# Kernel optimization log

Hardware: AMD Instinct MI355X
Metric: run time of the kernel (lower is better)

Reference implementation:

```python
import jax, jax.numpy as jnp
import numpy as np

# BiDiGemma (Aveygo/SRNext) wrapping RecurrentGemma-style ResidualBlocks:
#   block0 = RECURRENT (causal conv width 4 + RG-LRU linear recurrence)
#   block1 = local (sliding-window, MQA) ATTENTION with partial RoPE
# Dropout(0.1) is treated as eval-mode identity.

B, S, D, H = 4, 4096, 256, 4
HD = D // H            # head dim = 64
E = 3 * D              # mlp_expanded_width = expand_ratio * dim
W_ATT = D              # attention_window_size = dim = 256 (divides S)
TW = 4                 # recurrentgemma temporal conv width
_NEG = -2.3819763e38   # recurrentgemma masking constant

_PNAMES = ["ln_gamma","ln_beta","proj_w","proj_b","fconv_w","fconv_b","bconv_w","bconv_b",
 "rn0_t","rn0_c","ly_w","ly_b","lx_w","lx_b","lo_w","lo_b","c1d_w","c1d_b",
 "a_param","ig_w","ig_b","ag_w","ag_b","mlp0_up_w","mlp0_up_b","mlp0_dn_w","mlp0_dn_b",
 "rn1_t","rn1_c","q_w","k_w","v_w","o_w","o_b","mlp1_up_w","mlp1_up_b","mlp1_dn_w","mlp1_dn_b"]


def _init_params(key):
    ks = iter(jax.random.split(key, 24))
    nrm = lambda shape, s: jax.random.normal(next(ks), shape, jnp.float32) * s
    p = {}
    p["ln_gamma"] = jnp.ones((D,), jnp.float32); p["ln_beta"] = jnp.zeros((D,), jnp.float32)
    p["proj_w"] = nrm((D, D), D ** -0.5);  p["proj_b"] = jnp.zeros((D,), jnp.float32)
    p["fconv_w"] = nrm((D, D), D ** -0.5); p["fconv_b"] = jnp.zeros((D,), jnp.float32)
    p["bconv_w"] = nrm((D, D), D ** -0.5); p["bconv_b"] = jnp.zeros((D,), jnp.float32)
    p["rn0_t"] = jnp.zeros((D,), jnp.float32); p["rn0_c"] = jnp.zeros((D,), jnp.float32)
    p["ly_w"] = nrm((D, D), D ** -0.5); p["ly_b"] = jnp.zeros((D,), jnp.float32)
    p["lx_w"] = nrm((D, D), D ** -0.5); p["lx_b"] = jnp.zeros((D,), jnp.float32)
    p["lo_w"] = nrm((D, D), D ** -0.5); p["lo_b"] = jnp.zeros((D,), jnp.float32)
    p["c1d_w"] = nrm((TW, D), 0.1);     p["c1d_b"] = jnp.zeros((D,), jnp.float32)
    p["a_param"] = jnp.log(jnp.expm1(jnp.linspace(0.9, 1.5, D, dtype=jnp.float32)))
    p["ig_w"] = nrm((H, HD, HD), HD ** -0.5); p["ig_b"] = jnp.zeros((H, HD), jnp.float32)
    p["ag_w"] = nrm((H, HD, HD), HD ** -0.5); p["ag_b"] = jnp.zeros((H, HD), jnp.float32)
    p["mlp0_up_w"] = nrm((2, D, E), D ** -0.5); p["mlp0_up_b"] = jnp.zeros((2, E), jnp.float32)
    p["mlp0_dn_w"] = nrm((E, D), E ** -0.5);    p["mlp0_dn_b"] = jnp.zeros((D,), jnp.float32)
    p["rn1_t"] = jnp.zeros((D,), jnp.float32); p["rn1_c"] = jnp.zeros((D,), jnp.float32)
    p["q_w"] = nrm((D, D), D ** -0.5); p["k_w"] = nrm((D, HD), D ** -0.5); p["v_w"] = nrm((D, HD), D ** -0.5)
    p["o_w"] = nrm((D, D), D ** -0.5); p["o_b"] = jnp.zeros((D,), jnp.float32)
    p["mlp1_up_w"] = nrm((2, D, E), D ** -0.5); p["mlp1_up_b"] = jnp.zeros((2, E), jnp.float32)
    p["mlp1_dn_w"] = nrm((E, D), E ** -0.5);    p["mlp1_dn_b"] = jnp.zeros((D,), jnp.float32)
    return p


def _gelu(x):
    return jax.nn.gelu(x, approximate=False)  # torch F.gelu default (erf)


def _rms_norm(x, scale, eps=1e-6):
    var = jnp.mean(jnp.square(x), axis=-1, keepdims=True)
    return x * jax.lax.rsqrt(var + eps) * (1.0 + scale)


def _layer_norm(x, g, b, eps=1e-5):
    m = jnp.mean(x, axis=-1, keepdims=True)
    v = jnp.mean(jnp.square(x - m), axis=-1, keepdims=True)
    return (x - m) * jax.lax.rsqrt(v + eps) * g + b


def _block_diag(x, w, b):
    # BlockDiagonalLinear: per-head [HD x HD] blocks
    xh = x.reshape(*x.shape[:-1], H, HD)
    y = jnp.einsum('bshd,hdk->bshk', xh, w) + b
    return y.reshape(*x.shape)


def _causal_conv1d(x, w, b):
    # depthwise causal conv, w: [TW, D], w[TW-1] multiplies current token
    xp = jnp.pad(x, ((0, 0), (TW - 1, 0), (0, 0)))
    out = sum(xp[:, i:i + x.shape[1], :] * w[i] for i in range(TW))
    return out + b


def _rg_lru(x, pos, a_param, ig_w, ig_b, ag_w, ag_b):
    gate_x = jax.nn.sigmoid(_block_diag(x, ig_w, ig_b))
    gate_a = jax.nn.sigmoid(_block_diag(x, ag_w, ag_b))
    log_a = -8.0 * gate_a * jax.nn.softplus(a_param)   # c = 8
    a = jnp.exp(log_a)
    mult = jnp.sqrt(-jnp.expm1(2.0 * log_a))           # sqrt(1 - a^2)
    reset = (pos == 0)[..., None]
    mult = jnp.where(reset, 1.0, mult)
    bterm = x * gate_x * mult
    def comb(e1, e2):
        a1, b1 = e1
        a2, b2 = e2
        return a1 * a2, a2 * b1 + b2
    _, h = jax.lax.associative_scan(comb, (a, bterm), axis=1)
    return h


def _rope(x, pos):
    # partial RoPE: applied to first half of head dim (recurrentgemma)
    rot, rest = jnp.split(x, 2, axis=-1)
    f = rot.shape[-1] // 2
    inv_freq = 10000.0 ** (-(2.0 / rot.shape[-1]) * jnp.arange(f, dtype=jnp.float32))
    t = pos[..., None, None].astype(jnp.float32) * inv_freq  # [b, s, 1, f]
    sin, cos = jnp.sin(t), jnp.cos(t)
    x1, x2 = jnp.split(rot, 2, axis=-1)
    return jnp.concatenate([x1 * cos - x2 * sin, x2 * cos + x1 * sin, rest], axis=-1)


def _local_attention(x, pos, q_w, k_w, v_w, o_w, o_b):
    # MQA sliding-window attention, window = W_ATT; chunked to honor locality
    b, s, _ = x.shape
    q = (x @ q_w).reshape(b, s, H, HD)
    k = (x @ k_w).reshape(b, s, 1, HD)
    v = (x @ v_w).reshape(b, s, HD)
    q = _rope(q, pos) * (HD ** -0.5)
    k = _rope(k, pos)[:, :, 0]
    Wn = W_ATT
    nb = s // Wn
    qc = q.reshape(b, nb, Wn, H, HD)
    kp = jnp.pad(k, ((0, 0), (Wn, 0), (0, 0))).reshape(b, nb + 1, Wn, HD)
    vp = jnp.pad(v, ((0, 0), (Wn, 0), (0, 0))).reshape(b, nb + 1, Wn, HD)
    kc = jnp.concatenate([kp[:, :-1], kp[:, 1:]], axis=2)  # [b, nb, 2W, HD]
    vc = jnp.concatenate([vp[:, :-1], vp[:, 1:]], axis=2)
    logits = jnp.einsum('bnqhd,bnkd->bnhqk', qc, kc)
    i = jnp.arange(Wn)[:, None]
    j = jnp.arange(2 * Wn)[None, :]
    diff = (i + Wn) - j                       # q_pos - k_pos
    base = (diff >= 0) & (diff <= Wn)         # causal & q <= k + window_size
    cidx = jnp.arange(nb)[:, None, None]
    mask = base[None] & ((cidx > 0) | (j[None] >= Wn))  # no left padding in chunk 0
    logits = jnp.where(mask[None, :, None], logits, _NEG)
    probs = jax.nn.softmax(logits, axis=-1)
    out = jnp.einsum('bnhqk,bnkd->bnqhd', probs, vc).reshape(b, s, D)
    return out @ o_w + o_b


def _mlp(x, up_w, up_b, dn_w, dn_b):
    up = jnp.einsum('bsd,cde->cbse', x, up_w) + up_b[:, None, None, :]
    act = _gelu(up[0]) * up[1]
    return act @ dn_w + dn_b


def _gemma_block(x, pos, p):
    # ResidualBlock 0: RECURRENT
    raw = x
    xn = _rms_norm(raw, p['rn0_t'])
    y = _gelu(xn @ p['ly_w'] + p['ly_b'])
    xr = xn @ p['lx_w'] + p['lx_b']
    xr = _causal_conv1d(xr, p['c1d_w'], p['c1d_b'])
    xr = _rg_lru(xr, pos, p['a_param'], p['ig_w'], p['ig_b'], p['ag_w'], p['ag_b'])
    xr = (xr * y) @ p['lo_w'] + p['lo_b']
    residual = xr + raw
    x = _rms_norm(residual, p['rn0_c'])
    x = _mlp(x, p['mlp0_up_w'], p['mlp0_up_b'], p['mlp0_dn_w'], p['mlp0_dn_b']) + residual
    # ResidualBlock 1: local ATTENTION
    raw = x
    xn = _rms_norm(raw, p['rn1_t'])
    xa = _local_attention(xn, pos, p['q_w'], p['k_w'], p['v_w'], p['o_w'], p['o_b'])
    residual = xa + raw
    x = _rms_norm(residual, p['rn1_c'])
    x = _mlp(x, p['mlp1_up_w'], p['mlp1_up_b'], p['mlp1_dn_w'], p['mlp1_dn_b']) + residual
    return x


def _forward(skip, *params):
    p = dict(zip(_PNAMES, params))
    b, s, _ = skip.shape
    pos = jnp.broadcast_to(jnp.arange(s, dtype=jnp.int32)[None], (b, s))
    x = _layer_norm(skip, p['ln_gamma'], p['ln_beta']) @ p['proj_w'] + p['proj_b']
    z = jax.nn.sigmoid(jnp.mean(jax.nn.silu(skip), axis=-1, keepdims=True))
    fwd = _gemma_block(x @ p['fconv_w'] + p['fconv_b'], pos, p)  # Conv1d k=1 == pointwise
    bwd = _gemma_block(x @ p['bconv_w'] + p['bconv_b'], pos, p)
    return z * (fwd + bwd) + skip


def setup_inputs() -> dict:
    key = jax.random.key(0)
    kx, kp = jax.random.split(key)
    inp = {"skip": jax.random.normal(kx, (B, S, D), jnp.float32)}
    inp.update(_init_params(kp))
    return inp


def reference(skip, ln_gamma, ln_beta, proj_w, proj_b, fconv_w, fconv_b, bconv_w, bconv_b, rn0_t, rn0_c, ly_w, ly_b, lx_w, lx_b, lo_w, lo_b, c1d_w, c1d_b, a_param, ig_w, ig_b, ag_w, ag_b, mlp0_up_w, mlp0_up_b, mlp0_dn_w, mlp0_dn_b, rn1_t, rn1_c, q_w, k_w, v_w, o_w, o_b, mlp1_up_w, mlp1_up_b, mlp1_dn_w, mlp1_dn_b):
    return _forward(skip, ln_gamma, ln_beta, proj_w, proj_b, fconv_w, fconv_b, bconv_w, bconv_b, rn0_t, rn0_c, ly_w, ly_b, lx_w, lx_b, lo_w, lo_b, c1d_w, c1d_b, a_param, ig_w, ig_b, ag_w, ag_b, mlp0_up_w, mlp0_up_b, mlp0_dn_w, mlp0_dn_b, rn1_t, rn1_c, q_w, k_w, v_w, o_w, o_b, mlp1_up_w, mlp1_up_b, mlp1_dn_w, mlp1_dn_b)
```

## Files before the change

### kernel.cpp

```cpp
#include <hip/hip_runtime.h>
#include <math.h>
#include <stddef.h>


#define BB   4
#define SS   4096
#define DD   256
#define HH   4
#define HDIM 64
#define EE   768
#define RR   (BB*SS)
#define RR2  (2*RR)
#define WNN  256
#define CH   64
#define NCH  (SS/CH)

typedef __attribute__((ext_vector_type(8))) short bfrag;
typedef __attribute__((ext_vector_type(4))) float f4acc;

__device__ __forceinline__ float geluf(float x){
  float u = 1.5957691216f*(x + 0.044715f*x*x*x);
  float e = __expf(u);
  float t = 1.f - 2.f/(e+1.f);
  return 0.5f*x*(1.f+t);
}
__device__ __forceinline__ float sigm(float x){ return 1.0f/(1.0f+expf(-x)); }

__device__ __forceinline__ unsigned short f2bf(float x){
  unsigned u = __float_as_uint(x);
  return (unsigned short)((u + 0x7FFFu + ((u>>16)&1u)) >> 16);
}
__device__ __forceinline__ float bf2f(unsigned short h){
  return __uint_as_float(((unsigned)h) << 16);
}
__device__ __forceinline__ void split2(float v, unsigned short* h, unsigned short* l){
  unsigned short hb = f2bf(v);
  *h = hb; *l = f2bf(v - bf2f(hb));
}

__device__ __forceinline__ float wredSum(float v){
#pragma unroll
  for(int o=32;o>0;o>>=1) v += __shfl_xor(v,o,64);
  return v;
}

__global__ __launch_bounds__(256) void ln_z_k(const float* __restrict__ skip,
    const float* __restrict__ g, const float* __restrict__ b,
    unsigned short* __restrict__ oh, unsigned short* __restrict__ ol,
    float* __restrict__ z)
{
  int row  = blockIdx.x*4 + (threadIdx.x>>6);
  int lane = threadIdx.x & 63;
  float4 v = ((const float4*)(skip + (size_t)row*DD))[lane];
  float s  = v.x+v.y+v.z+v.w;
  float sq = v.x*v.x+v.y*v.y+v.z*v.z+v.w*v.w;
  float si = v.x*sigm(v.x)+v.y*sigm(v.y)+v.z*sigm(v.z)+v.w*sigm(v.w);
  s = wredSum(s); sq = wredSum(sq); si = wredSum(si);
  float mean = s*(1.0f/DD);
  float var  = sq*(1.0f/DD) - mean*mean;
  float inv  = rsqrtf(var + 1e-5f);
  float4 gv = ((const float4*)g)[lane];
  float4 bv = ((const float4*)b)[lane];
  float o0 = (v.x-mean)*inv*gv.x + bv.x;
  float o1 = (v.y-mean)*inv*gv.y + bv.y;
  float o2 = (v.z-mean)*inv*gv.z + bv.z;
  float o3 = (v.w-mean)*inv*gv.w + bv.w;
  ushort4 hi, lo;
  split2(o0,&hi.x,&lo.x); split2(o1,&hi.y,&lo.y);
  split2(o2,&hi.z,&lo.z); split2(o3,&hi.w,&lo.w);
  ((ushort4*)(oh + (size_t)row*DD))[lane] = hi;
  ((ushort4*)(ol + (size_t)row*DD))[lane] = lo;
  if(lane==0) z[row] = sigm(si*(1.0f/DD));
}

__global__ __launch_bounds__(256) void rms_k(const float* __restrict__ x,
    const float* __restrict__ t,
    unsigned short* __restrict__ oh, unsigned short* __restrict__ ol)
{
  int row  = blockIdx.x*4 + (threadIdx.x>>6);
  int lane = threadIdx.x & 63;
  float4 v = ((const float4*)(x + (size_t)row*DD))[lane];
  float sq = v.x*v.x+v.y*v.y+v.z*v.z+v.w*v.w;
  sq = wredSum(sq);
  float inv = rsqrtf(sq*(1.0f/DD) + 1e-6f);
  float4 tv = ((const float4*)t)[lane];
  float o0 = v.x*inv*(1.0f+tv.x);
  float o1 = v.y*inv*(1.0f+tv.y);
  float o2 = v.z*inv*(1.0f+tv.z);
  float o3 = v.w*inv*(1.0f+tv.w);
  ushort4 hi, lo;
  split2(o0,&hi.x,&lo.x); split2(o1,&hi.y,&lo.y);
  split2(o2,&hi.z,&lo.z); split2(o3,&hi.w,&lo.w);
  ((ushort4*)(oh + (size_t)row*DD))[lane] = hi;
  ((ushort4*)(ol + (size_t)row*DD))[lane] = lo;
}

struct TS  { const float* s; unsigned short* h; unsigned short* l; int K; int N; };
struct TS8 { TS t[8]; };

__global__ __launch_bounds__(256) void tsplit8_k(TS8 g){
  TS tt = g.t[blockIdx.y];
  int idx = blockIdx.x*256 + threadIdx.x;
  int tot = tt.K*tt.N;
  if(idx >= tot) return;
  int k = idx / tt.N;
  int n = idx - k*tt.N;
  float x = tt.s[idx];
  unsigned short hb = f2bf(x);
  unsigned short lb = f2bf(x - bf2f(hb));
  tt.h[(size_t)n*tt.K + k] = hb;
  tt.l[(size_t)n*tt.K + k] = lb;
}

template<int BN, int MODE, int DUAL, int OUT, int TERMS>
__global__ __launch_bounds__(256) void gemm_mfma(
    const unsigned short* __restrict__ Ah_g, const unsigned short* __restrict__ Al_g,
    const unsigned short* __restrict__ B0h, const unsigned short* __restrict__ B0l,
    const unsigned short* __restrict__ B1h, const unsigned short* __restrict__ B1l,
    const float* __restrict__ bias0, const float* __restrict__ bias1,
    const float* __restrict__ Res, float* __restrict__ C,
    unsigned short* __restrict__ Ch, unsigned short* __restrict__ Cl,
    int K, int lda, int ldc)
{
  constexpr int NT = BN/32;
  constexpr int ST = 40;
  __shared__ unsigned short Ash[128*ST];
  __shared__ unsigned short Asl[TERMS==3 ? 128*ST : 8];
  __shared__ unsigned short Bsh[BN*ST];
  __shared__ unsigned short Bsl[TERMS>=2 ? BN*ST : 8];
  __shared__ unsigned short B2h[DUAL?BN*ST:8];
  __shared__ unsigned short B2l[(DUAL && TERMS>=2)?BN*ST:8];

  const int tid  = threadIdx.x;
  const int lane = tid & 63, wave = tid >> 6;
  const int wm = wave >> 1, wn = wave & 1;
  const int bm = blockIdx.y*128, bn = blockIdx.x*BN;
  const int m16 = lane & 15, q = lane >> 4;

  f4acc acc[4][NT];
  f4acc acc2[DUAL?4:1][DUAL?NT:1];
#pragma unroll
  for(int i=0;i<4;i++)
#pragma unroll
    for(int j=0;j<NT;j++){
      acc[i][j] = (f4acc)0.f;
      if constexpr(DUAL) acc2[i][j] = (f4acc)0.f;
    }

  const int r0 = tid >> 2, c0 = tid & 3;
  const int coff = c0*8;
  const int d0 = r0*ST + coff, d1 = (r0+64)*ST + coff;

  const unsigned short* pAh0 = Ah_g + (size_t)(bm+r0)*lda + coff;
  const unsigned short* pAh1 = pAh0 + (size_t)64*lda;
  const unsigned short* pAl0 = (TERMS==3) ? (Al_g + (size_t)(bm+r0)*lda + coff)
                                          : (const unsigned short*)nullptr;
  const unsigned short* pAl1 = (TERMS==3) ? (pAl0 + (size_t)64*lda)
                                          : (const unsigned short*)nullptr;
  const unsigned short *pB0h0=nullptr,*pB0h1=nullptr,*pB0l0=nullptr,*pB0l1=nullptr;
  const unsigned short *pBa=nullptr,*pBb=nullptr,*pBc=nullptr,*pBd=nullptr;
  if constexpr(BN==128){
    pB0h0 = B0h + (size_t)(bn+r0)*K + coff;  pB0h1 = pB0h0 + (size_t)64*K;
    if constexpr(TERMS>=2){
      pB0l0 = B0l + (size_t)(bn+r0)*K + coff;  pB0l1 = pB0l0 + (size_t)64*K;
    }
  } else {
    pBa = B0h + (size_t)(bn+r0)*K + coff;
    if constexpr(TERMS>=2) pBb = B0l + (size_t)(bn+r0)*K + coff;
    if constexpr(DUAL){
      pBc = B1h + (size_t)(bn+r0)*K + coff;
      if constexpr(TERMS>=2) pBd = B1l + (size_t)(bn+r0)*K + coff;
    }
  }

  for(int k0 = 0; k0 < K; k0 += 32){
    *(float4*)&Ash[d0] = *(const float4*)(pAh0 + k0);
    *(float4*)&Ash[d1] = *(const float4*)(pAh1 + k0);
    if constexpr(TERMS==3){
      *(float4*)&Asl[d0] = *(const float4*)(pAl0 + k0);
      *(float4*)&Asl[d1] = *(const float4*)(pAl1 + k0);
    }
    if constexpr(BN==128){
      *(float4*)&Bsh[d0] = *(const float4*)(pB0h0 + k0);
      *(float4*)&Bsh[d1] = *(const float4*)(pB0h1 + k0);
      if constexpr(TERMS>=2){
        *(float4*)&Bsl[d0] = *(const float4*)(pB0l0 + k0);
        *(float4*)&Bsl[d1] = *(const float4*)(pB0l1 + k0);
      }
    } else {
      *(float4*)&Bsh[d0] = *(const float4*)(pBa + k0);
      if constexpr(TERMS>=2) *(float4*)&Bsl[d0] = *(const float4*)(pBb + k0);
      if constexpr(DUAL){
        *(float4*)&B2h[d0] = *(const float4*)(pBc + k0);
        if constexpr(TERMS>=2) *(float4*)&B2l[d0] = *(const float4*)(pBd + k0);
      }
    }
    __syncthreads();

    bfrag ah[4], al[TERMS==3?4:1], b0hf[NT], b0lf[TERMS>=2?NT:1];
    bfrag b1hf[DUAL?NT:1], b1lf[(DUAL&&TERMS>=2)?NT:1];
#pragma unroll
    for(int mi=0;mi<4;mi++){
      int row = wm*64 + mi*16 + m16;
      ah[mi] = *(const bfrag*)&Ash[row*ST + q*8];
      if constexpr(TERMS==3) al[mi] = *(const bfrag*)&Asl[row*ST + q*8];
    }
#pragma unroll
    for(int ni=0;ni<NT;ni++){
      int n = wn*(BN/2) + ni*16 + m16;
      b0hf[ni] = *(const bfrag*)&Bsh[n*ST + q*8];
      if constexpr(TERMS>=2) b0lf[ni] = *(const bfrag*)&Bsl[n*ST + q*8];
      if constexpr(DUAL){
        b1hf[ni] = *(const bfrag*)&B2h[n*ST + q*8];
        if constexpr(TERMS>=2) b1lf[ni] = *(const bfrag*)&B2l[n*ST + q*8];
      }
    }
#pragma unroll
    for(int mi=0;mi<4;mi++)
#pragma unroll
      for(int ni=0;ni<NT;ni++){
        acc[mi][ni] = __builtin_amdgcn_mfma_f32_16x16x32_bf16(ah[mi], b0hf[ni], acc[mi][ni],0,0,0);
        if constexpr(TERMS>=2)
          acc[mi][ni] = __builtin_amdgcn_mfma_f32_16x16x32_bf16(ah[mi], b0lf[ni], acc[mi][ni],0,0,0);
        if constexpr(TERMS==3)
          acc[mi][ni] = __builtin_amdgcn_mfma_f32_16x16x32_bf16(al[mi], b0hf[ni], acc[mi][ni],0,0,0);
        if constexpr(DUAL){
          acc2[mi][ni] = __builtin_amdgcn_mfma_f32_16x16x32_bf16(ah[mi], b1hf[ni], acc2[mi][ni],0,0,0);
          if constexpr(TERMS>=2)
            acc2[mi][ni] = __builtin_amdgcn_mfma_f32_16x16x32_bf16(ah[mi], b1lf[ni], acc2[mi][ni],0,0,0);
          if constexpr(TERMS==3)
            acc2[mi][ni] = __builtin_amdgcn_mfma_f32_16x16x32_bf16(al[mi], b1hf[ni], acc2[mi][ni],0,0,0);
        }
      }
    __syncthreads();
  }

  if constexpr(OUT==0 || OUT==1 || OUT==5){
#pragma unroll
    for(int ni=0;ni<NT;ni++){
      const int col = bn + wn*(BN/2) + ni*16 + m16;
      float bv0 = (MODE&1) ? bias0[col] : 0.f;
      float bv1 = DUAL ? bias1[col] : 0.f;
#pragma unroll
      for(int mi=0;mi<4;mi++){
#pragma unroll
        for(int r=0;r<4;r++){
          const int row = bm + wm*64 + mi*16 + q*4 + r;
          float v = acc[mi][ni][r] + bv0;
          if constexpr(DUAL){
            float v2 = acc2[mi][ni][r] + bv1;
            v = geluf(v) * v2;
          } else if(MODE&2){
            v = geluf(v);
          }
          if(MODE&8) v += Res[(size_t)row*ldc + col];
          if constexpr(OUT==0){
            C[(size_t)row*ldc + col] = v;
          } else if constexpr(OUT==1){
            unsigned short hb = f2bf(v);
            Ch[(size_t)row*ldc + col] = hb;
            Cl[(size_t)row*ldc + col] = f2bf(v - bf2f(hb));
          } else {
            Ch[(size_t)row*ldc + col] = f2bf(v);
          }
        }
      }
    }
  } else if constexpr(OUT==2){
    const int hb = bn + wn*64;
    const float p = (float)m16;
    const float invf = __expf(-p * 0.575646273248511f);
#pragma unroll
    for(int mi=0;mi<4;mi++){
#pragma unroll
      for(int r=0;r<4;r++){
        const int row = bm + wm*64 + mi*16 + q*4 + r;
        const int s = row & (SS-1);
        float t = (float)s * invf;
        float sn, cs; __sincosf(t, &sn, &cs);
        float x1 = acc[mi][0][r], x2 = acc[mi][1][r];
        float v0 = (x1*cs - x2*sn)*0.125f;
        float v1 = (x2*cs + x1*sn)*0.125f;
        float v2 = acc[mi][2][r]*0.125f;
        float v3 = acc[mi][3][r]*0.125f;
        size_t base = (size_t)row*ldc + hb;
        unsigned short hh;
        hh=f2bf(v0); Ch[base+m16]=hh;    Cl[base+m16]   =f2bf(v0-bf2f(hh));
        hh=f2bf(v1); Ch[base+16+m16]=hh; Cl[base+16+m16]=f2bf(v1-bf2f(hh));
        hh=f2bf(v2); Ch[base+32+m16]=hh; Cl[base+32+m16]=f2bf(v2-bf2f(hh));
        hh=f2bf(v3); Ch[base+48+m16]=hh; Cl[base+48+m16]=f2bf(v3-bf2f(hh));
      }
    }
  } else if constexpr(OUT==3){
    const float p = (float)m16;
    const float invf = __expf(-p * 0.575646273248511f);
#pragma unroll
    for(int mi=0;mi<4;mi++){
#pragma unroll
      for(int r=0;r<4;r++){
        const int row = bm + wm*64 + mi*16 + q*4 + r;
        const int s = row & (SS-1);
        float v0, v1;
        if(wn==0){
          float t = (float)s * invf;
          float sn, cs; __sincosf(t, &sn, &cs);
          float x1 = acc[mi][0][r], x2 = acc[mi][1][r];
          v0 = x1*cs - x2*sn;
          v1 = x2*cs + x1*sn;
        } else {
          v0 = acc[mi][0][r]; v1 = acc[mi][1][r];
        }
        size_t base = (size_t)row*ldc + wn*32;
        unsigned short hh;
        hh=f2bf(v0); Ch[base+m16]=hh;    Cl[base+m16]   =f2bf(v0-bf2f(hh));
        hh=f2bf(v1); Ch[base+16+m16]=hh; Cl[base+16+m16]=f2bf(v1-bf2f(hh));
      }
    }
  } else if constexpr(OUT==4){
#pragma unroll
    for(int ni=0;ni<NT;ni++){
      const int col = wn*32 + ni*16 + m16;
#pragma unroll
      for(int mi=0;mi<4;mi++){
        const int rowb = bm + wm*64 + mi*16 + q*4;
        const int b = rowb >> 12, sl = rowb & (SS-1);
        ushort4 hv;
        hv.x = f2bf(acc[mi][ni][0]); hv.y = f2bf(acc[mi][ni][1]);
        hv.z = f2bf(acc[mi][ni][2]); hv.w = f2bf(acc[mi][ni][3]);
        *(ushort4*)(Ch + ((size_t)(b*64 + col))*SS + sl) = hv;
      }
    }
  }
}

__global__ __launch_bounds__(256) void gates_k(
    const float* __restrict__ X,
    const float* __restrict__ igw, const float* __restrict__ igb,
    const float* __restrict__ agw, const float* __restrict__ agb,
    const float* __restrict__ ap,
    float* __restrict__ Aout, float* __restrict__ Bout)
{
  constexpr int BK = 16;
  __shared__ float Ask[BK][132];
  __shared__ float Bi[BK][68];
  __shared__ float Ba[BK][68];

  const int h  = blockIdx.y;
  const int bm = blockIdx.x*128;
  const int tid = threadIdx.x;
  const int tx = tid & 15, ty = tid >> 4;
  const int r0 = tid >> 2, c0 = (tid & 3)*4;
  const int br = tid >> 4, bc = (tid & 15)*4;

  const float* Xb = X + (size_t)h*HDIM;
  const float* wI = igw + (size_t)h*HDIM*HDIM;
  const float* wA = agw + (size_t)h*HDIM*HDIM;

  float accI[8][4], accA[8][4];
#pragma unroll
  for(int i=0;i<8;i++)
#pragma unroll
    for(int j=0;j<4;j++){ accI[i][j]=0.f; accA[i][j]=0.f; }

  for(int k0=0;k0<HDIM;k0+=BK){
#pragma unroll
    for(int hf=0;hf<2;hf++){
      float4 av = *(const float4*)(Xb + (size_t)(bm+r0+hf*64)*DD + (k0+c0));
      Ask[c0+0][r0+hf*64]=av.x; Ask[c0+1][r0+hf*64]=av.y;
      Ask[c0+2][r0+hf*64]=av.z; Ask[c0+3][r0+hf*64]=av.w;
    }
    *(float4*)&Bi[br][bc] = *(const float4*)(wI + (size_t)(k0+br)*HDIM + bc);
    *(float4*)&Ba[br][bc] = *(const float4*)(wA + (size_t)(k0+br)*HDIM + bc);
    __syncthreads();
#pragma unroll
    for(int k=0;k<BK;k++){
      float a[8];
      *(float4*)&a[0] = *(const float4*)&Ask[k][ty*8];
      *(float4*)&a[4] = *(const float4*)&Ask[k][ty*8+4];
      float bi[4], ba[4];
      *(float4*)&bi[0] = *(const float4*)&Bi[k][tx*4];
      *(float4*)&ba[0] = *(const float4*)&Ba[k][tx*4];
#pragma unroll
      for(int i=0;i<8;i++)
#pragma unroll
        for(int j=0;j<4;j++){
          accI[i][j] = fmaf(a[i], bi[j], accI[i][j]);
          accA[i][j] = fmaf(a[i], ba[j], accA[i][j]);
        }
    }
    __syncthreads();
  }

  const int colg = h*HDIM + tx*4;
  const float4 bI  = *(const float4*)(igb + colg);
  const float4 bA  = *(const float4*)(agb + colg);
  const float4 apv = *(const float4*)(ap  + colg);
  const float* bIf = (const float*)&bI;
  const float* bAf = (const float*)&bA;
  const float* apf = (const float*)&apv;
  float spv[4];
#pragma unroll
  for(int j=0;j<4;j++)
    spv[j] = (apf[j] > 20.f) ? apf[j] : log1pf(expf(apf[j]));

#pragma unroll
  for(int i=0;i<8;i++){
    const int row = bm + ty*8 + i;
    const int s = row & (SS-1);
    const float4 xv = *(const float4*)(X + (size_t)row*DD + colg);
    const float* xf = (const float*)&xv;
    float oa[4], ob[4];
#pragma unroll
    for(int j=0;j<4;j++){
      float gx = sigm(accI[i][j] + bIf[j]);
      float ga = sigm(accA[i][j] + bAf[j]);
      float la = -8.f * ga * spv[j];
      float a_ = expf(la);
      float mult = (s==0) ? 1.f : sqrtf(fmaxf(-expm1f(2.f*la), 0.f));
      oa[j] = a_;
      ob[j] = xf[j] * gx * mult;
    }
    *(float4*)(Aout + (size_t)row*DD + colg) = *(const float4*)oa;
    *(float4*)(Bout + (size_t)row*DD + colg) = *(const float4*)ob;
  }
}

__global__ __launch_bounds__(256) void conv_k(const float* __restrict__ x,
    const float* __restrict__ w, const float* __restrict__ b, float* __restrict__ out)
{
  int idx = blockIdx.x*256 + threadIdx.x;
  int d = idx & (DD-1);
  int r = idx >> 8;
  int s = r & (SS-1);
  float acc = b[d];
#pragma unroll
  for(int i=0;i<4;i++){
    int t = s - 3 + i;
    if(t >= 0) acc += w[i*DD + d] * x[(size_t)(r-3+i)*DD + d];
  }
  out[idx] = acc;
}

__global__ __launch_bounds__(256) void scan1_k(const float* __restrict__ A,
    const float* __restrict__ Bv, float* __restrict__ csa, float* __restrict__ csb)
{
  int idx = blockIdx.x*256 + threadIdx.x;
  int d = idx & (DD-1);
  int c = (idx >> 8) & (NCH-1);
  int b = idx >> 14;
  size_t base = ((size_t)b*SS + (size_t)c*CH)*DD + d;
  float Aa = 1.f, Bb_ = 0.f;
  for(int t=0;t<CH;t++){
    float a  = A [base + (size_t)t*DD];
    float bb = Bv[base + (size_t)t*DD];
    Aa  = a*Aa;
    Bb_ = a*Bb_ + bb;
  }
  csa[idx] = Aa; csb[idx] = Bb_;
}

__global__ __launch_bounds__(256) void scan2_k(const float* __restrict__ csa,
    float* __restrict__ csb)
{
  int idx = blockIdx.x*256 + threadIdx.x;
  int d = idx & (DD-1);
  int b = idx >> 8;
  float h = 0.f;
  for(int c=0;c<NCH;c++){
    size_t i = ((size_t)b*NCH + c)*DD + d;
    float Aa = csa[i], Bb_ = csb[i];
    csb[i] = h;
    h = Aa*h + Bb_;
  }
}

__global__ __launch_bounds__(256) void scan3_k(const float* __restrict__ A,
    const float* __restrict__ Bv, const float* __restrict__ csb,
    const unsigned short* __restrict__ Yh,
    unsigned short* __restrict__ Hh, unsigned short* __restrict__ Hl)
{
  int idx = blockIdx.x*256 + threadIdx.x;
  int d = idx & (DD-1);
  int c = (idx >> 8) & (NCH-1);
  int b = idx >> 14;
  size_t base = ((size_t)b*SS + (size_t)c*CH)*DD + d;
  float h = csb[idx];
  for(int t=0;t<CH;t++){
    float a  = A [base + (size_t)t*DD];
    float bb = Bv[base + (size_t)t*DD];
    h = a*h + bb;
    float v = h * bf2f(Yh[base + (size_t)t*DD]);
    unsigned short hb = f2bf(v);
    Hh[base + (size_t)t*DD] = hb;
    Hl[base + (size_t)t*DD] = f2bf(v - bf2f(hb));
  }
}

#define AST 72
__global__ __launch_bounds__(256) void attn_k(
    const unsigned short* __restrict__ Qh, const unsigned short* __restrict__ Ql,
    const unsigned short* __restrict__ Kh, const unsigned short* __restrict__ Kl,
    const unsigned short* __restrict__ Vt,
    unsigned short* __restrict__ Oh, unsigned short* __restrict__ Ol)
{
  __shared__ unsigned short Ksh[64*AST], Ksl[64*AST], Vsh[64*AST];
  __shared__ unsigned short Ps[4*16*AST];

  const int qt = blockIdx.x & 3, n = blockIdx.x >> 2;
  const int h = blockIdx.y, b = blockIdx.z;
  const int tid = threadIdx.x;
  const int lane = tid & 63, w = tid >> 6;
  const int m16 = lane & 15, q = lane >> 4;
  const int s0 = n*WNN + qt*64;

  const size_t qro = ((size_t)(b*SS + s0 + w*16 + m16))*DD + h*HDIM + q*8;
  bfrag qh0 = *(const bfrag*)(Qh + qro);
  bfrag qh1 = *(const bfrag*)(Qh + qro + 32);
  bfrag ql0 = *(const bfrag*)(Ql + qro);
  bfrag ql1 = *(const bfrag*)(Ql + qro + 32);

  float mrow[4], lrow[4];
  f4acc oacc[4];
#pragma unroll
  for(int i=0;i<4;i++){ mrow[i]=-3.0e38f; lrow[i]=0.f; oacc[i]=(f4acc)0.f; }

  const int ktlo = (n==0) ? 4 : qt;
  const int kthi = qt + 4;
  const int sr = tid >> 2, sc = tid & 3;

  for(int kt=ktlo; kt<=kthi; kt++){
    const int kbase = (n-1)*WNN + kt*64;
#pragma unroll
    for(int cc=0; cc<2; cc++){
      int g = sc + cc*4;
      *(float4*)&Ksh[sr*AST + g*8] =
        *(const float4*)(Kh + (size_t)(b*SS + kbase + sr)*HDIM + g*8);
      *(float4*)&Ksl[sr*AST + g*8] =
        *(const float4*)(Kl + (size_t)(b*SS + kbase + sr)*HDIM + g*8);
      *(float4*)&Vsh[sr*AST + g*8] =
        *(const float4*)(Vt + ((size_t)(b*64 + sr))*SS + kbase + g*8);
    }
    __syncthreads();

    f4acc sacc[4];
#pragma unroll
    for(int nt=0;nt<4;nt++) sacc[nt] = (f4acc)0.f;
#pragma unroll
    for(int nt=0;nt<4;nt++){
      const int kr = (nt*16+m16)*AST;
      bfrag kh0 = *(const bfrag*)&Ksh[kr + q*8];
      bfrag kh1 = *(const bfrag*)&Ksh[kr + 32 + q*8];
      bfrag kl0 = *(const bfrag*)&Ksl[kr + q*8];
      bfrag kl1 = *(const bfrag*)&Ksl[kr + 32 + q*8];
      sacc[nt] = __builtin_amdgcn_mfma_f32_16x16x32_bf16(qh0, kh0, sacc[nt],0,0,0);
      sacc[nt] = __builtin_amdgcn_mfma_f32_16x16x32_bf16(qh0, kl0, sacc[nt],0,0,0);
      sacc[nt] = __builtin_amdgcn_mfma_f32_16x16x32_bf16(ql0, kh0, sacc[nt],0,0,0);
      sacc[nt] = __builtin_amdgcn_mfma_f32_16x16x32_bf16(qh1, kh1, sacc[nt],0,0,0);
      sacc[nt] = __builtin_amdgcn_mfma_f32_16x16x32_bf16(qh1, kl1, sacc[nt],0,0,0);
      sacc[nt] = __builtin_amdgcn_mfma_f32_16x16x32_bf16(ql1, kh1, sacc[nt],0,0,0);
    }

    const bool needlo = (kt == qt+4);
    const bool needhi = (kt == qt);
#pragma unroll
    for(int r=0;r<4;r++){
      int qp = qt*64 + w*16 + q*4 + r;
      float sv[4];
      float tm = -3.0e38f;
#pragma unroll
      for(int nt=0;nt<4;nt++){
        float scv = sacc[nt][r];
        if(needlo || needhi){
          int kj = kt*64 + nt*16 + m16;
          int diff = qp + WNN - kj;
          bool ok = (!needlo || diff >= 0) && (!needhi || diff <= WNN);
          scv = ok ? scv : -3.0e38f;
        }
        sv[nt] = scv;
        tm = fmaxf(tm, scv);
      }
#pragma unroll
      for(int off=1; off<16; off<<=1) tm = fmaxf(tm, __shfl_xor(tm, off, 64));
      float mn = fmaxf(mrow[r], tm);
      float alpha = __expf(mrow[r]-mn);
      float rs = 0.f;
#pragma unroll
      for(int nt=0;nt<4;nt++){
        float pp = __expf(sv[nt]-mn);
        rs += pp;
        Ps[w*16*AST + (q*4+r)*AST + nt*16 + m16] = f2bf(pp);
      }
#pragma unroll
      for(int off=1; off<16; off<<=1) rs += __shfl_xor(rs, off, 64);
      lrow[r] = lrow[r]*alpha + rs;
      mrow[r] = mn;
#pragma unroll
      for(int nt=0;nt<4;nt++) oacc[nt][r] *= alpha;
    }

#pragma unroll
    for(int s=0;s<2;s++){
      bfrag pa = *(const bfrag*)&Ps[w*16*AST + m16*AST + s*32 + q*8];
#pragma unroll
      for(int nt=0;nt<4;nt++){
        bfrag vh_ = *(const bfrag*)&Vsh[(nt*16+m16)*AST + s*32 + q*8];
        oacc[nt] = __builtin_amdgcn_mfma_f32_16x16x32_bf16(pa, vh_, oacc[nt],0,0,0);
      }
    }
    __syncthreads();
  }

#pragma unroll
  for(int r=0;r<4;r++){
    float invl = 1.f/lrow[r];
    const size_t rowbase = ((size_t)(b*SS + s0 + w*16 + q*4 + r))*DD + h*HDIM;
#pragma unroll
    for(int nt=0;nt<4;nt++){
      float v = oacc[nt][r]*invl;
      unsigned short hb = f2bf(v);
      Oh[rowbase + nt*16 + m16] = hb;
      Ol[rowbase + nt*16 + m16] = f2bf(v - bf2f(hb));
    }
  }
}

__global__ __launch_bounds__(256) void comb_k(const float* __restrict__ of,
    const float* __restrict__ ob, const float* __restrict__ z,
    const float* __restrict__ skip, float* __restrict__ out)
{
  int idx = blockIdx.x*256 + threadIdx.x;
  int r = idx >> 8;
  out[idx] = z[r]*(of[idx]+ob[idx]) + skip[idx];
}

struct Params {
  const float *ln_gamma,*ln_beta,*proj_w,*proj_b,*fconv_w,*fconv_b,*bconv_w,*bconv_b,
    *rn0_t,*rn0_c,*ly_w,*ly_b,*lx_w,*lx_b,*lo_w,*lo_b,*c1d_w,*c1d_b,*a_param,
    *ig_w,*ig_b,*ag_w,*ag_b,*mlp0_up_w,*mlp0_up_b,*mlp0_dn_w,*mlp0_dn_b,
    *rn1_t,*rn1_c,*q_w,*k_w,*v_w,*o_w,*o_b,*mlp1_up_w,*mlp1_up_b,*mlp1_dn_w,*mlp1_dn_b;
};

struct WSplit {
  unsigned short *proj_h,*proj_l,*fconv_h,*fconv_l,*bconv_h,*bconv_l,
    *ly_h,*ly_l,*lx_h,*lx_l,*lo_h,*lo_l,*q_h,*q_l,*o_h,*o_l,
    *k_h,*k_l,*v_h,*v_l,
    *up0a_h,*up0a_l,*up0b_h,*up0b_l,*up1a_h,*up1a_l,*up1b_h,*up1b_l,
    *dn0_h,*dn0_l,*dn1_h,*dn1_l;
};

#define USN ((unsigned short*)nullptr)

extern "C" void kernel_launch(void* const* d_in, const int* in_sizes, int n_in,
                              void* d_out, int out_size, void* d_ws, size_t ws_size,
                              hipStream_t stream)
{
  (void)in_sizes; (void)n_in; (void)out_size; (void)ws_size;
  const float* skip = (const float*)d_in[0];
  Params p;
  p.ln_gamma  =(const float*)d_in[1];  p.ln_beta  =(const float*)d_in[2];
  p.proj_w    =(const float*)d_in[3];  p.proj_b   =(const float*)d_in[4];
  p.fconv_w   =(const float*)d_in[5];  p.fconv_b  =(const float*)d_in[6];
  p.bconv_w   =(const float*)d_in[7];  p.bconv_b  =(const float*)d_in[8];
  p.rn0_t     =(const float*)d_in[9];  p.rn0_c    =(const float*)d_in[10];
  p.ly_w      =(const float*)d_in[11]; p.ly_b     =(const float*)d_in[12];
  p.lx_w      =(const float*)d_in[13]; p.lx_b     =(const float*)d_in[14];
  p.lo_w      =(const float*)d_in[15]; p.lo_b     =(const float*)d_in[16];
  p.c1d_w     =(const float*)d_in[17]; p.c1d_b    =(const float*)d_in[18];
  p.a_param   =(const float*)d_in[19];
  p.ig_w      =(const float*)d_in[20]; p.ig_b     =(const float*)d_in[21];
  p.ag_w      =(const float*)d_in[22]; p.ag_b     =(const float*)d_in[23];
  p.mlp0_up_w =(const float*)d_in[24]; p.mlp0_up_b=(const float*)d_in[25];
  p.mlp0_dn_w =(const float*)d_in[26]; p.mlp0_dn_b=(const float*)d_in[27];
  p.rn1_t     =(const float*)d_in[28]; p.rn1_c    =(const float*)d_in[29];
  p.q_w       =(const float*)d_in[30]; p.k_w      =(const float*)d_in[31];
  p.v_w       =(const float*)d_in[32]; p.o_w      =(const float*)d_in[33];
  p.o_b       =(const float*)d_in[34];
  p.mlp1_up_w =(const float*)d_in[35]; p.mlp1_up_b=(const float*)d_in[36];
  p.mlp1_dn_w =(const float*)d_in[37]; p.mlp1_dn_b=(const float*)d_in[38];

  float* ws = (float*)d_ws;
  const size_t RD  = (size_t)RR*DD;
  const size_t PD2 = (size_t)RR2*DD;
  size_t off = 0;
  float* Z   = ws + off; off += 16384;
  float* XB2 = ws + off; off += 2*RD;
  float* CV2 = ws + off; off += 2*RD;
  float* W1  = ws + off; off += 2*RD;
  float* W2  = ws + off; off += 2*RD;
  float* W3  = ws + off; off += RD;
  float* W4  = ws + off; off += 2*RD;

  float* CSA = CV2;
  float* CSB = CV2 + 8*NCH*DD;

  unsigned short* NPh = (unsigned short*)W4;  unsigned short* NPl = NPh + PD2;
  unsigned short* HYh = NPh;                  unsigned short* HYl = NPl;
  unsigned short* X0h = (unsigned short*)W1;  unsigned short* X0l = X0h + (size_t)RR*DD;
  float* XR2 = W1;
  unsigned short* Qph = (unsigned short*)W1;  unsigned short* Qpl = Qph + PD2;
  float* Abuf = W2;
  unsigned short* P2h = (unsigned short*)W2;  unsigned short* P2l = P2h + PD2;
  unsigned short* Yh  = (unsigned short*)W3;
  unsigned short* KPh = (unsigned short*)W3;  unsigned short* KPl = KPh + (size_t)RR2*HDIM;
  unsigned short* Vt  = KPl + (size_t)RR2*HDIM;
  unsigned short* ACTh = (unsigned short*)W1;
  float* OUT2 = XB2;

  unsigned short* sp = (unsigned short*)(ws + off);
  WSplit w;
  auto alloc_s = [&](size_t n){ unsigned short* r = sp; sp += n; return r; };
  const size_t SDD = (size_t)DD*DD, SKV = (size_t)DD*HDIM, SUP = (size_t)DD*EE;
  w.proj_h=alloc_s(SDD);  w.proj_l=alloc_s(SDD);
  w.fconv_h=alloc_s(SDD); w.fconv_l=alloc_s(SDD);
  w.bconv_h=alloc_s(SDD); w.bconv_l=alloc_s(SDD);
  w.ly_h=alloc_s(SDD);    w.ly_l=alloc_s(SDD);
  w.lx_h=alloc_s(SDD);    w.lx_l=alloc_s(SDD);
  w.lo_h=alloc_s(SDD);    w.lo_l=alloc_s(SDD);
  w.q_h=alloc_s(SDD);     w.q_l=alloc_s(SDD);
  w.o_h=alloc_s(SDD);     w.o_l=alloc_s(SDD);
  w.k_h=alloc_s(SKV);     w.k_l=alloc_s(SKV);
  w.v_h=alloc_s(SKV);     w.v_l=alloc_s(SKV);
  w.up0a_h=alloc_s(SUP);  w.up0a_l=alloc_s(SUP);
  w.up0b_h=alloc_s(SUP);  w.up0b_l=alloc_s(SUP);
  w.up1a_h=alloc_s(SUP);  w.up1a_l=alloc_s(SUP);
  w.up1b_h=alloc_s(SUP);  w.up1b_l=alloc_s(SUP);
  w.dn0_h=alloc_s(SUP);   w.dn0_l=alloc_s(SUP);
  w.dn1_h=alloc_s(SUP);   w.dn1_l=alloc_s(SUP);

  dim3 blk(256);
  dim3 g2(2,128,1);
  dim3 g2m(2,256,1), g64m(1,256,1), gdual(12,256,1);
  dim3 ggate(RR2/128, HH, 1);

  {
    TS8 ga;
    ga.t[0] = {p.proj_w,  w.proj_h,  w.proj_l,  DD, DD};
    ga.t[1] = {p.fconv_w, w.fconv_h, w.fconv_l, DD, DD};
    ga.t[2] = {p.bconv_w, w.bconv_h, w.bconv_l, DD, DD};
    ga.t[3] = {p.ly_w,    w.ly_h,    w.ly_l,    DD, DD};
    ga.t[4] = {p.lx_w,    w.lx_h,    w.lx_l,    DD, DD};
    ga.t[5] = {p.lo_w,    w.lo_h,    w.lo_l,    DD, DD};
    ga.t[6] = {p.q_w,     w.q_h,     w.q_l,     DD, DD};
    ga.t[7] = {p.o_w,     w.o_h,     w.o_l,     DD, DD};
    tsplit8_k<<<dim3(DD*DD/256, 8), blk, 0, stream>>>(ga);
    TS8 gb;
    gb.t[0] = {p.k_w,              w.k_h,    w.k_l,    DD, HDIM};
    gb.t[1] = {p.v_w,              w.v_h,    w.v_l,    DD, HDIM};
    gb.t[2] = {p.mlp0_up_w,        w.up0a_h, w.up0a_l, DD, EE};
    gb.t[3] = {p.mlp0_up_w+(size_t)DD*EE, w.up0b_h, w.up0b_l, DD, EE};
    gb.t[4] = {p.mlp1_up_w,        w.up1a_h, w.up1a_l, DD, EE};
    gb.t[5] = {p.mlp1_up_w+(size_t)DD*EE, w.up1b_h, w.up1b_l, DD, EE};
    gb.t[6] = {p.mlp0_dn_w,        w.dn0_h,  w.dn0_l,  EE, DD};
    gb.t[7] = {p.mlp1_dn_w,        w.dn1_h,  w.dn1_l,  EE, DD};
    tsplit8_k<<<dim3(DD*EE/256, 8), blk, 0, stream>>>(gb);
  }

  ln_z_k<<<RR/4, blk, 0, stream>>>(skip, p.ln_gamma, p.ln_beta, NPh, NPl, Z);
  gemm_mfma<128,1,0,1,3><<<g2,blk,0,stream>>>(NPh,NPl, w.proj_h,w.proj_l, USN,USN,
      p.proj_b,nullptr,nullptr, nullptr, X0h, X0l, DD,DD,DD);
  gemm_mfma<128,1,0,0,3><<<g2,blk,0,stream>>>(X0h,X0l, w.fconv_h,w.fconv_l, USN,USN,
      p.fconv_b,nullptr,nullptr, XB2, USN,USN, DD,DD,DD);
  gemm_mfma<128,1,0,0,3><<<g2,blk,0,stream>>>(X0h,X0l, w.bconv_h,w.bconv_l, USN,USN,
      p.bconv_b,nullptr,nullptr, XB2 + RD, USN,USN, DD,DD,DD);

  rms_k<<<RR2/4, blk, 0, stream>>>(XB2, p.rn0_t, NPh, NPl);
  gemm_mfma<128,3,0,5,2><<<g2m,blk,0,stream>>>(NPh,USN, w.ly_h,w.ly_l, USN,USN,
      p.ly_b,nullptr,nullptr, nullptr, Yh, USN, DD,DD,DD);
  gemm_mfma<128,1,0,0,2><<<g2m,blk,0,stream>>>(NPh,USN, w.lx_h,w.lx_l, USN,USN,
      p.lx_b,nullptr,nullptr, XR2, USN,USN, DD,DD,DD);
  conv_k<<<(size_t)RR2*DD/256, blk, 0, stream>>>(XR2, p.c1d_w, p.c1d_b, CV2);
  gates_k<<<ggate,blk,0,stream>>>(CV2, p.ig_w, p.ig_b, p.ag_w, p.ag_b,
      p.a_param, Abuf, XR2);
  scan1_k<<<8*NCH*DD/256, blk,0,stream>>>(Abuf, XR2, CSA, CSB);
  scan2_k<<<8*DD/256, blk,0,stream>>>(CSA, CSB);
  scan3_k<<<8*NCH*DD/256, blk,0,stream>>>(Abuf, XR2, CSB, Yh, HYh, HYl);
  gemm_mfma<128,9,0,0,2><<<g2m,blk,0,stream>>>(HYh,USN, w.lo_h,w.lo_l, USN,USN,
      p.lo_b,nullptr, XB2, CV2, USN,USN, DD,DD,DD);
  rms_k<<<RR2/4,blk,0,stream>>>(CV2, p.rn0_c, NPh, NPl);
  gemm_mfma<64,1,1,5,1><<<gdual,blk,0,stream>>>(NPh,USN, w.up0a_h,USN,
      w.up0b_h,USN, p.mlp0_up_b, p.mlp0_up_b+EE, nullptr, nullptr,
      ACTh, USN, DD,DD,EE);
  gemm_mfma<128,9,0,0,2><<<g2m,blk,0,stream>>>(ACTh,USN, w.dn0_h,w.dn0_l, USN,USN,
      p.mlp0_dn_b,nullptr, CV2, XB2, USN,USN, EE,EE,DD);

  rms_k<<<RR2/4,blk,0,stream>>>(XB2, p.rn1_t, NPh, NPl);
  gemm_mfma<128,0,0,2,2><<<g2m,blk,0,stream>>>(NPh,USN, w.q_h,w.q_l, USN,USN,
      nullptr,nullptr,nullptr, nullptr, Qph, Qpl, DD,DD,DD);
  gemm_mfma<64,0,0,3,3><<<g64m,blk,0,stream>>>(NPh,NPl, w.k_h,w.k_l, USN,USN,
      nullptr,nullptr,nullptr, nullptr, KPh, KPl, DD,DD,HDIM);
  gemm_mfma<64,0,0,4,3><<<g64m,blk,0,stream>>>(NPh,NPl, w.v_h,w.v_l, USN,USN,
      nullptr,nullptr,nullptr, nullptr, Vt, USN, DD,DD,HDIM);
  attn_k<<<dim3(64,4,8),blk,0,stream>>>(Qph, Qpl, KPh, KPl, Vt, P2h, P2l);
  gemm_mfma<128,9,0,0,2><<<g2m,blk,0,stream>>>(P2h,USN, w.o_h,w.o_l, USN,USN,
      p.o_b,nullptr, XB2, CV2, USN,USN, DD,DD,DD);
  rms_k<<<RR2/4,blk,0,stream>>>(CV2, p.rn1_c, NPh, NPl);
  gemm_mfma<64,1,1,5,1><<<gdual,blk,0,stream>>>(NPh,USN, w.up1a_h,USN,
      w.up1b_h,USN, p.mlp1_up_b, p.mlp1_up_b+EE, nullptr, nullptr,
      ACTh, USN, DD,DD,EE);
  gemm_mfma<128,9,0,0,2><<<g2m,blk,0,stream>>>(ACTh,USN, w.dn1_h,w.dn1_l, USN,USN,
      p.mlp1_dn_b,nullptr, CV2, OUT2, USN,USN, EE,EE,DD);

  comb_k<<<RR*DD/256, blk, 0, stream>>>(OUT2, OUT2 + RD, Z, skip, (float*)d_out);
}
```

Baseline: 785.9 us.

## Move RG-LRU gate projections to bf16 split-precision MFMA

Replaces the FP32 FMA gate GEMM with an MFMA kernel that uses hi/lo bf16 splits (three products per pair) for the per-head input and a-gate projections. The conv kernel now writes its output straight into bf16 hi/lo buffers, and the gate weights are pre-split and transposed by an extra tsplit launch. This aims to cut the scalar-FMA compute cost of the gates. In exchange it adds split/convert traffic, writes Aout/Bout as scalar non-vectorized stores, and uses fast __expf in place of expm1f, which may shift accuracy slightly.

```diff
diff --git a/kernel.cpp b/kernel.cpp
--- a/kernel.cpp
+++ b/kernel.cpp
@@ -333,100 +333,9 @@
   }
 }
 
-__global__ __launch_bounds__(256) void gates_k(
-    const float* __restrict__ X,
-    const float* __restrict__ igw, const float* __restrict__ igb,
-    const float* __restrict__ agw, const float* __restrict__ agb,
-    const float* __restrict__ ap,
-    float* __restrict__ Aout, float* __restrict__ Bout)
-{
-  constexpr int BK = 16;
-  __shared__ float Ask[BK][132];
-  __shared__ float Bi[BK][68];
-  __shared__ float Ba[BK][68];
-
-  const int h  = blockIdx.y;
-  const int bm = blockIdx.x*128;
-  const int tid = threadIdx.x;
-  const int tx = tid & 15, ty = tid >> 4;
-  const int r0 = tid >> 2, c0 = (tid & 3)*4;
-  const int br = tid >> 4, bc = (tid & 15)*4;
-
-  const float* Xb = X + (size_t)h*HDIM;
-  const float* wI = igw + (size_t)h*HDIM*HDIM;
-  const float* wA = agw + (size_t)h*HDIM*HDIM;
-
-  float accI[8][4], accA[8][4];
-#pragma unroll
-  for(int i=0;i<8;i++)
-#pragma unroll
-    for(int j=0;j<4;j++){ accI[i][j]=0.f; accA[i][j]=0.f; }
-
-  for(int k0=0;k0<HDIM;k0+=BK){
-#pragma unroll
-    for(int hf=0;hf<2;hf++){
-      float4 av = *(const float4*)(Xb + (size_t)(bm+r0+hf*64)*DD + (k0+c0));
-      Ask[c0+0][r0+hf*64]=av.x; Ask[c0+1][r0+hf*64]=av.y;
-      Ask[c0+2][r0+hf*64]=av.z; Ask[c0+3][r0+hf*64]=av.w;
-    }
-    *(float4*)&Bi[br][bc] = *(const float4*)(wI + (size_t)(k0+br)*HDIM + bc);
-    *(float4*)&Ba[br][bc] = *(const float4*)(wA + (size_t)(k0+br)*HDIM + bc);
-    __syncthreads();
-#pragma unroll
-    for(int k=0;k<BK;k++){
-      float a[8];
-      *(float4*)&a[0] = *(const float4*)&Ask[k][ty*8];
-      *(float4*)&a[4] = *(const float4*)&Ask[k][ty*8+4];
-      float bi[4], ba[4];
-      *(float4*)&bi[0] = *(const float4*)&Bi[k][tx*4];
-      *(float4*)&ba[0] = *(const float4*)&Ba[k][tx*4];
-#pragma unroll
-      for(int i=0;i<8;i++)
-#pragma unroll
-        for(int j=0;j<4;j++){
-          accI[i][j] = fmaf(a[i], bi[j], accI[i][j]);
-          accA[i][j] = fmaf(a[i], ba[j], accA[i][j]);
-        }
-    }
-    __syncthreads();
-  }
-
-  const int colg = h*HDIM + tx*4;
-  const float4 bI  = *(const float4*)(igb + colg);
-  const float4 bA  = *(const float4*)(agb + colg);
-  const float4 apv = *(const float4*)(ap  + colg);
-  const float* bIf = (const float*)&bI;
-  const float* bAf = (const float*)&bA;
-  const float* apf = (const float*)&apv;
-  float spv[4];
-#pragma unroll
-  for(int j=0;j<4;j++)
-    spv[j] = (apf[j] > 20.f) ? apf[j] : log1pf(expf(apf[j]));
-
-#pragma unroll
-  for(int i=0;i<8;i++){
-    const int row = bm + ty*8 + i;
-    const int s = row & (SS-1);
-    const float4 xv = *(const float4*)(X + (size_t)row*DD + colg);
-    const float* xf = (const float*)&xv;
-    float oa[4], ob[4];
-#pragma unroll
-    for(int j=0;j<4;j++){
-      float gx = sigm(accI[i][j] + bIf[j]);
-      float ga = sigm(accA[i][j] + bAf[j]);
-      float la = -8.f * ga * spv[j];
-      float a_ = expf(la);
-      float mult = (s==0) ? 1.f : sqrtf(fmaxf(-expm1f(2.f*la), 0.f));
-      oa[j] = a_;
-      ob[j] = xf[j] * gx * mult;
-    }
-    *(float4*)(Aout + (size_t)row*DD + colg) = *(const float4*)oa;
-    *(float4*)(Bout + (size_t)row*DD + colg) = *(const float4*)ob;
-  }
-}
-
-__global__ __launch_bounds__(256) void conv_k(const float* __restrict__ x,
-    const float* __restrict__ w, const float* __restrict__ b, float* __restrict__ out)
+__global__ __launch_bounds__(256) void conv_split_k(const float* __restrict__ x,
+    const float* __restrict__ w, const float* __restrict__ b,
+    unsigned short* __restrict__ oh, unsigned short* __restrict__ ol)
 {
   int idx = blockIdx.x*256 + threadIdx.x;
   int d = idx & (DD-1);
@@ -438,7 +347,102 @@
     int t = s - 3 + i;
     if(t >= 0) acc += w[i*DD + d] * x[(size_t)(r-3+i)*DD + d];
   }
-  out[idx] = acc;
+  unsigned short hb = f2bf(acc);
+  oh[idx] = hb;
+  ol[idx] = f2bf(acc - bf2f(hb));
+}
+
+__global__ __launch_bounds__(256) void gates_mfma_k(
+    const unsigned short* __restrict__ Xh, const unsigned short* __restrict__ Xl,
+    const unsigned short* __restrict__ igth, const unsigned short* __restrict__ igtl,
+    const unsigned short* __restrict__ agth, const unsigned short* __restrict__ agtl,
+    const float* __restrict__ igb, const float* __restrict__ agb,
+    const float* __restrict__ ap,
+    float* __restrict__ Aout, float* __restrict__ Bout)
+{
+  constexpr int ST = 72;
+  __shared__ unsigned short Ash[128*ST];
+  __shared__ unsigned short Asl[128*ST];
+
+  const int h  = blockIdx.x;
+  const int bm = blockIdx.y*128;
+  const int tid = threadIdx.x;
+  const int lane = tid & 63, wave = tid >> 6;
+  const int wm = wave >> 1, wn = wave & 1;
+  const int m16 = lane & 15, q = lane >> 4;
+
+  {
+    const int r = tid >> 1, kq = (tid & 1)*32;
+    const size_t src = (size_t)(bm + r)*DD + h*HDIM + kq;
+    const int dst = r*ST + kq;
+#pragma unroll
+    for(int i=0;i<4;i++){
+      *(float4*)&Ash[dst + i*8] = *(const float4*)(Xh + src + i*8);
+      *(float4*)&Asl[dst + i*8] = *(const float4*)(Xl + src + i*8);
+    }
+  }
+  __syncthreads();
+
+  f4acc accI[4][2], accA[4][2];
+#pragma unroll
+  for(int i=0;i<4;i++)
+#pragma unroll
+    for(int j=0;j<2;j++){ accI[i][j]=(f4acc)0.f; accA[i][j]=(f4acc)0.f; }
+
+  const size_t wbase = (size_t)h*HDIM*HDIM;
+#pragma unroll
+  for(int ks=0;ks<2;ks++){
+    bfrag ah[4], al[4];
+#pragma unroll
+    for(int mi=0;mi<4;mi++){
+      const int row = wm*64 + mi*16 + m16;
+      ah[mi] = *(const bfrag*)&Ash[row*ST + ks*32 + q*8];
+      al[mi] = *(const bfrag*)&Asl[row*ST + ks*32 + q*8];
+    }
+#pragma unroll
+    for(int ni=0;ni<2;ni++){
+      const size_t bo = wbase + (size_t)(wn*32 + ni*16 + m16)*HDIM + ks*32 + q*8;
+      bfrag bIh = *(const bfrag*)(igth + bo);
+      bfrag bIl = *(const bfrag*)(igtl + bo);
+      bfrag bAh = *(const bfrag*)(agth + bo);
+      bfrag bAl = *(const bfrag*)(agtl + bo);
+#pragma unroll
+      for(int mi=0;mi<4;mi++){
+        accI[mi][ni] = __builtin_amdgcn_mfma_f32_16x16x32_bf16(ah[mi], bIh, accI[mi][ni],0,0,0);
+        accI[mi][ni] = __builtin_amdgcn_mfma_f32_16x16x32_bf16(ah[mi], bIl, accI[mi][ni],0,0,0);
+        accI[mi][ni] = __builtin_amdgcn_mfma_f32_16x16x32_bf16(al[mi], bIh, accI[mi][ni],0,0,0);
+        accA[mi][ni] = __builtin_amdgcn_mfma_f32_16x16x32_bf16(ah[mi], bAh, accA[mi][ni],0,0,0);
+        accA[mi][ni] = __builtin_amdgcn_mfma_f32_16x16x32_bf16(ah[mi], bAl, accA[mi][ni],0,0,0);
+        accA[mi][ni] = __builtin_amdgcn_mfma_f32_16x16x32_bf16(al[mi], bAh, accA[mi][ni],0,0,0);
+      }
+    }
+  }
+
+#pragma unroll
+  for(int ni=0;ni<2;ni++){
+    const int cl  = wn*32 + ni*16 + m16;
+    const int col = h*HDIM + cl;
+    const float bI = igb[col], bA = agb[col];
+    const float apv = ap[col];
+    const float sp = (apv > 20.f) ? apv : log1pf(expf(apv));
+#pragma unroll
+    for(int mi=0;mi<4;mi++){
+#pragma unroll
+      for(int r=0;r<4;r++){
+        const int lrow = wm*64 + mi*16 + q*4 + r;
+        const int row = bm + lrow;
+        const int s = row & (SS-1);
+        float gx = 1.f/(1.f + __expf(-(accI[mi][ni][r] + bI)));
+        float ga = 1.f/(1.f + __expf(-(accA[mi][ni][r] + bA)));
+        float la = -8.f * ga * sp;
+        float a_ = __expf(la);
+        float mult = (s==0) ? 1.f : sqrtf(fmaxf(1.f - __expf(2.f*la), 0.f));
+        float x = bf2f(Ash[lrow*ST + cl]) + bf2f(Asl[lrow*ST + cl]);
+        Aout[(size_t)row*DD + col] = a_;
+        Bout[(size_t)row*DD + col] = x * gx * mult;
+      }
+    }
+  }
 }
 
 __global__ __launch_bounds__(256) void scan1_k(const float* __restrict__ A,
@@ -645,7 +649,8 @@
     *ly_h,*ly_l,*lx_h,*lx_l,*lo_h,*lo_l,*q_h,*q_l,*o_h,*o_l,
     *k_h,*k_l,*v_h,*v_l,
     *up0a_h,*up0a_l,*up0b_h,*up0b_l,*up1a_h,*up1a_l,*up1b_h,*up1b_l,
-    *dn0_h,*dn0_l,*dn1_h,*dn1_l;
+    *dn0_h,*dn0_l,*dn1_h,*dn1_l,
+    *igt_h,*igt_l,*agt_h,*agt_l;
 };
 
 #define USN ((unsigned short*)nullptr)
@@ -695,6 +700,7 @@
 
   unsigned short* NPh = (unsigned short*)W4;  unsigned short* NPl = NPh + PD2;
   unsigned short* HYh = NPh;                  unsigned short* HYl = NPl;
+  unsigned short* CVh = NPh;                  unsigned short* CVl = NPl;
   unsigned short* X0h = (unsigned short*)W1;  unsigned short* X0l = X0h + (size_t)RR*DD;
   float* XR2 = W1;
   unsigned short* Qph = (unsigned short*)W1;  unsigned short* Qpl = Qph + PD2;
@@ -710,6 +716,7 @@
   WSplit w;
   auto alloc_s = [&](size_t n){ unsigned short* r = sp; sp += n; return r; };
   const size_t SDD = (size_t)DD*DD, SKV = (size_t)DD*HDIM, SUP = (size_t)DD*EE;
+  const size_t SBD = (size_t)HH*HDIM*HDIM;
   w.proj_h=alloc_s(SDD);  w.proj_l=alloc_s(SDD);
   w.fconv_h=alloc_s(SDD); w.fconv_l=alloc_s(SDD);
   w.bconv_h=alloc_s(SDD); w.bconv_l=alloc_s(SDD);
@@ -726,11 +733,13 @@
   w.up1b_h=alloc_s(SUP);  w.up1b_l=alloc_s(SUP);
   w.dn0_h=alloc_s(SUP);   w.dn0_l=alloc_s(SUP);
   w.dn1_h=alloc_s(SUP);   w.dn1_l=alloc_s(SUP);
+  w.igt_h=alloc_s(SBD);   w.igt_l=alloc_s(SBD);
+  w.agt_h=alloc_s(SBD);   w.agt_l=alloc_s(SBD);
 
   dim3 blk(256);
   dim3 g2(2,128,1);
   dim3 g2m(2,256,1), g64m(1,256,1), gdual(12,256,1);
-  dim3 ggate(RR2/128, HH, 1);
+  dim3 ggm(HH, RR2/128, 1);
 
   {
     TS8 ga;
@@ -753,6 +762,14 @@
     gb.t[6] = {p.mlp0_dn_w,        w.dn0_h,  w.dn0_l,  EE, DD};
     gb.t[7] = {p.mlp1_dn_w,        w.dn1_h,  w.dn1_l,  EE, DD};
     tsplit8_k<<<dim3(DD*EE/256, 8), blk, 0, stream>>>(gb);
+    TS8 gc;
+    for(int h=0;h<HH;h++){
+      gc.t[h]   = {p.ig_w + (size_t)h*HDIM*HDIM, w.igt_h + (size_t)h*HDIM*HDIM,
+                   w.igt_l + (size_t)h*HDIM*HDIM, HDIM, HDIM};
+      gc.t[4+h] = {p.ag_w + (size_t)h*HDIM*HDIM, w.agt_h + (size_t)h*HDIM*HDIM,
+                   w.agt_l + (size_t)h*HDIM*HDIM, HDIM, HDIM};
+    }
+    tsplit8_k<<<dim3(HDIM*HDIM/256, 8), blk, 0, stream>>>(gc);
   }
 
   ln_z_k<<<RR/4, blk, 0, stream>>>(skip, p.ln_gamma, p.ln_beta, NPh, NPl, Z);
@@ -768,9 +785,9 @@
       p.ly_b,nullptr,nullptr, nullptr, Yh, USN, DD,DD,DD);
   gemm_mfma<128,1,0,0,2><<<g2m,blk,0,stream>>>(NPh,USN, w.lx_h,w.lx_l, USN,USN,
       p.lx_b,nullptr,nullptr, XR2, USN,USN, DD,DD,DD);
-  conv_k<<<(size_t)RR2*DD/256, blk, 0, stream>>>(XR2, p.c1d_w, p.c1d_b, CV2);
-  gates_k<<<ggate,blk,0,stream>>>(CV2, p.ig_w, p.ig_b, p.ag_w, p.ag_b,
-      p.a_param, Abuf, XR2);
+  conv_split_k<<<(size_t)RR2*DD/256, blk, 0, stream>>>(XR2, p.c1d_w, p.c1d_b, CVh, CVl);
+  gates_mfma_k<<<ggm,blk,0,stream>>>(CVh, CVl, w.igt_h, w.igt_l, w.agt_h, w.agt_l,
+      p.ig_b, p.ag_b, p.a_param, Abuf, XR2);
   scan1_k<<<8*NCH*DD/256, blk,0,stream>>>(Abuf, XR2, CSA, CSB);
   scan2_k<<<8*DD/256, blk,0,stream>>>(CSA, CSB);
   scan3_k<<<8*NCH*DD/256, blk,0,stream>>>(Abuf, XR2, CSB, Yh, HYh, HYl);
```

Result: faster. 752.5 us (-4.3%).
